# Kernel tuning notes

Measured on AMD Instinct MI355X. Metric: run time of the kernel, lower is better.

Reference implementation:

```python
import jax, jax.numpy as jnp
import numpy as np


def setup_inputs() -> dict:
    key = jax.random.key(0)
    k1, k2 = jax.random.split(key)
    B, C, H, W = 8, 128, 96, 160
    x1 = jax.random.normal(k1, (B, C, H, W), dtype=jnp.float32)
    x2 = jax.random.normal(k2, (B, C, H, W), dtype=jnp.float32)
    return {"x1": x1, "x2": x2, "d": 4}


def reference(x1, x2, d):
    # x1, x2: (B, C, H, W); output: (B, (2d+1)^2, H, W)
    b, c, h, w = x1.shape
    x2p = jnp.pad(x2, ((0, 0), (0, 0), (d, d), (d, d)))
    # Loop over the small fixed (2d+1)^2 displacement set (81 for d=4);
    # each term is a channel-reduced elementwise product (shift-multiply-sum).
    corrs = [
        jnp.einsum("bchw,bchw->bhw", x1,
                   jax.lax.dynamic_slice(x2p, (0, 0, i, j), (b, c, h, w)))
        for i in range(2 * d + 1)
        for j in range(2 * d + 1)
    ]
    out = jnp.stack(corrs, axis=1)  # (B, (2d+1)^2, H, W)
    return out / c
```

## Files before the change

kernel.cpp:

```cpp
#include <hip/hip_runtime.h>
#include <stdint.h>

#define Bb 8
#define Cc 128
#define Hh 96
#define Ww 160
#define HW (Hh*Ww)
#define Kk 81

typedef __attribute__((ext_vector_type(8))) short short8;
typedef __attribute__((ext_vector_type(4))) float floatx4;
typedef __attribute__((ext_vector_type(4))) unsigned int uintx4;

__device__ __forceinline__ uint32_t bf16rne(float f) {
  uint32_t u = __float_as_uint(f);
  return (u + 0x7FFFu + ((u >> 16) & 1u)) >> 16;
}


__global__ __launch_bounds__(512, 4)
void corr_kernel(const float* __restrict__ x1, const float* __restrict__ x2,
                 float* __restrict__ out) {
  __shared__ __align__(16) ushort ldsX2[16*24*40];
  __shared__ __align__(16) ushort ldsX1[8*16*40];

  const int tid = threadIdx.x;
  const int flat = blockIdx.x;
  const int b  = flat & 7;
  const int j  = flat >> 3;
  const int by = j / 10;
  const int bx = j - by * 10;
  const int w0 = bx * 16;
  const int h0 = by * 8;

  const int lane = tid & 63;
  const int wv   = tid >> 6;
  const int vy = wv & 3, vx = wv >> 2;
  const int n = lane & 15, quad = lane >> 4;
  const int s = n >> 3, pw = n & 7;

  floatx4 acc[10];
#pragma unroll
  for (int t = 0; t < 10; ++t) acc[t] = (floatx4){0.f, 0.f, 0.f, 0.f};

  for (int ck = 0; ck < 4; ++ck) {
    const int c0 = ck * 32;
    if (ck) __syncthreads();

#pragma unroll
    for (int it = 0; it < 3; ++it) {
      int T   = it * 512 + tid;
      int w24 = T % 24;
      int t2  = T / 24;
      int rw  = t2 & 15;
      int cg  = t2 >> 4;
      int gh = h0 - 4 + rw;
      int gw = w0 - 4 + w24;
      bool ok = ((unsigned)gh < Hh) && ((unsigned)gw < Ww);
      const float* src = x2 + ((size_t)(b*Cc + c0 + cg*8) * HW + gh*Ww + gw);
      uint32_t p0, p1, p2, p3;
      {
        float a0 = ok ? src[0*HW] : 0.f;
        float a1 = ok ? src[1*HW] : 0.f;
        float a2 = ok ? src[2*HW] : 0.f;
        float a3 = ok ? src[3*HW] : 0.f;
        float a4 = ok ? src[4*HW] : 0.f;
        float a5 = ok ? src[5*HW] : 0.f;
        float a6 = ok ? src[6*HW] : 0.f;
        float a7 = ok ? src[7*HW] : 0.f;
        p0 = bf16rne(a0) | (bf16rne(a1) << 16);
        p1 = bf16rne(a2) | (bf16rne(a3) << 16);
        p2 = bf16rne(a4) | (bf16rne(a5) << 16);
        p3 = bf16rne(a6) | (bf16rne(a7) << 16);
      }
      *(uintx4*)&ldsX2[(rw*24 + w24)*40 + cg*8] = (uintx4){p0, p1, p2, p3};
    }

    {
      int T  = tid;
      int wl = T & 15;
      int t2 = T >> 4;
      int rl = t2 & 7;
      int cg = t2 >> 3;
      const float* src = x1 + ((size_t)(b*Cc + c0 + cg*8) * HW
                               + (h0 + rl)*Ww + (w0 + wl));
      uint32_t p0, p1, p2, p3;
      float a0 = src[0*HW], a1 = src[1*HW], a2 = src[2*HW], a3 = src[3*HW];
      float a4 = src[4*HW], a5 = src[5*HW], a6 = src[6*HW], a7 = src[7*HW];
      p0 = bf16rne(a0) | (bf16rne(a1) << 16);
      p1 = bf16rne(a2) | (bf16rne(a3) << 16);
      p2 = bf16rne(a4) | (bf16rne(a5) << 16);
      p3 = bf16rne(a6) | (bf16rne(a7) << 16);
      *(uintx4*)&ldsX1[(rl*16 + wl)*40 + cg*8] = (uintx4){p0, p1, p2, p3};
    }

    __syncthreads();

    short8 bfrag = *(const short8*)&ldsX1[((2*vy + s)*16 + 8*vx + pw)*40 + quad*8];
#pragma unroll
    for (int t = 0; t < 10; ++t) {
      short8 afrag = *(const short8*)&ldsX2[((2*vy + t)*24 + 8*vx + n)*40 + quad*8];
      acc[t] = __builtin_amdgcn_mfma_f32_16x16x32_bf16(afrag, bfrag, acc[t], 0, 0, 0);
    }
  }

  const float scale = 1.0f / 128.0f;
  const int ph  = h0 + 2*vy + s;
  const int pwg = w0 + 8*vx + pw;
#pragma unroll
  for (int t = 0; t < 10; ++t) {
    int di = t - 4 - s;
    if ((unsigned)(di + 4) > 8u) continue;
#pragma unroll
    for (int r = 0; r < 4; ++r) {
      int dj = quad*4 + r - 4 - pw;
      if ((unsigned)(dj + 4) > 8u) continue;
      int kk = (di + 4) * 9 + (dj + 4);
      out[((size_t)b*Kk + kk) * HW + ph*Ww + pwg] = acc[t][r] * scale;
    }
  }
}

extern "C" void kernel_launch(void* const* d_in, const int* in_sizes, int n_in,
                              void* d_out, int out_size, void* d_ws, size_t ws_size,
                              hipStream_t stream) {
  const float* x1 = (const float*)d_in[0];
  const float* x2 = (const float*)d_in[1];
  float* out = (float*)d_out;
  corr_kernel<<<dim3(960, 1, 1), dim3(512, 1, 1), 0, stream>>>(x1, x2, out);
}
```

Baseline: 187.0 us.

## Pre-transpose inputs to bf16 channel-last in workspace, then correlate directly from global

Adds a transpose kernel that converts x1 and x2 from NCHW fp32 into NHWC bf16 in the workspace. A new correlation kernel then loads MFMA fragments straight from global memory as contiguous 16-byte channel vectors, without LDS staging or barriers. This removes the strided per-channel loads and repeated bf16 conversion of halo data in every block. In exchange it adds a second launch and a full extra read and write pass over both inputs. The path runs only when the workspace is large enough and otherwise falls back to the old kernel.

```diff
diff --git a/kernel.cpp b/kernel.cpp
--- a/kernel.cpp
+++ b/kernel.cpp
@@ -1,5 +1,6 @@
 #include <hip/hip_runtime.h>
 #include <stdint.h>
+#include <stddef.h>
 
 #define Bb 8
 #define Cc 128
@@ -17,6 +18,100 @@
   return (u + 0x7FFFu + ((u >> 16) & 1u)) >> 16;
 }
 
+
+#define TPX 32
+__global__ __launch_bounds__(256)
+void transpose_kernel(const float* __restrict__ x1, const float* __restrict__ x2,
+                      ushort* __restrict__ x1t, ushort* __restrict__ x2t) {
+  __shared__ float lds[TPX * 130];
+  const int t   = threadIdx.x;
+  const int b   = blockIdx.y;
+  const int hw0 = blockIdx.x * TPX;
+  const float* src = blockIdx.z ? x2 : x1;
+  ushort*      dst = blockIdx.z ? x2t : x1t;
+
+  const int p4 = t & 7;
+  const int cb = t >> 3;
+#pragma unroll
+  for (int i = 0; i < 4; ++i) {
+    const int c = cb + i * 32;
+    floatx4 v = *(const floatx4*)&src[(size_t)(b * Cc + c) * HW + hw0 + p4 * 4];
+#pragma unroll
+    for (int jj = 0; jj < 4; ++jj)
+      lds[(p4 * 4 + jj) * 130 + c] = v[jj];
+  }
+  __syncthreads();
+
+  const int px = t >> 3;
+#pragma unroll
+  for (int i = 0; i < 2; ++i) {
+    const int k = (t & 7) + 8 * i;
+    const float* row = &lds[px * 130 + k * 8];
+    uint32_t q0 = bf16rne(row[0]) | (bf16rne(row[1]) << 16);
+    uint32_t q1 = bf16rne(row[2]) | (bf16rne(row[3]) << 16);
+    uint32_t q2 = bf16rne(row[4]) | (bf16rne(row[5]) << 16);
+    uint32_t q3 = bf16rne(row[6]) | (bf16rne(row[7]) << 16);
+    *(uintx4*)&dst[((size_t)b * HW + hw0 + px) * Cc + k * 8] = (uintx4){q0, q1, q2, q3};
+  }
+}
+
+__global__ __launch_bounds__(512)
+void corr_t_kernel(const ushort* __restrict__ x1t, const ushort* __restrict__ x2t,
+                   float* __restrict__ out) {
+  const int tid  = threadIdx.x;
+  const int flat = blockIdx.x;
+  const int b  = flat & 7;
+  const int j  = flat >> 3;
+  const int by = j / 10;
+  const int bx = j - by * 10;
+  const int w0 = bx * 16;
+  const int h0 = by * 8;
+
+  const int lane = tid & 63;
+  const int wv   = tid >> 6;
+  const int vy = wv & 3, vx = wv >> 2;
+  const int n = lane & 15, quad = lane >> 4;
+  const int s = n >> 3, pw = n & 7;
+
+  floatx4 acc[10];
+#pragma unroll
+  for (int t = 0; t < 10; ++t) acc[t] = (floatx4){0.f, 0.f, 0.f, 0.f};
+
+  const int gw2  = w0 - 4 + 8 * vx + n;
+  const bool okw = (unsigned)gw2 < (unsigned)Ww;
+  const int gh2b = h0 - 4 + 2 * vy;
+  const long p2  = ((long)b * HW + (long)gh2b * Ww + gw2) * Cc;
+  const long p1  = ((long)b * HW + (long)(h0 + 2 * vy + s) * Ww
+                    + (w0 + 8 * vx + pw)) * Cc;
+
+#pragma unroll
+  for (int ck = 0; ck < 4; ++ck) {
+    const short8 bfrag = *(const short8*)&x1t[p1 + ck * 32 + quad * 8];
+#pragma unroll
+    for (int t = 0; t < 10; ++t) {
+      short8 afrag = (short8){0, 0, 0, 0, 0, 0, 0, 0};
+      if (okw && (unsigned)(gh2b + t) < (unsigned)Hh)
+        afrag = *(const short8*)&x2t[p2 + (long)t * (Ww * Cc) + ck * 32 + quad * 8];
+      acc[t] = __builtin_amdgcn_mfma_f32_16x16x32_bf16(afrag, bfrag, acc[t], 0, 0, 0);
+    }
+  }
+
+  const float scale = 1.0f / 128.0f;
+  const int ph  = h0 + 2 * vy + s;
+  const int pwg = w0 + 8 * vx + pw;
+#pragma unroll
+  for (int t = 0; t < 10; ++t) {
+    int di = t - 4 - s;
+    if ((unsigned)(di + 4) > 8u) continue;
+#pragma unroll
+    for (int r = 0; r < 4; ++r) {
+      int dj = quad * 4 + r - 4 - pw;
+      if ((unsigned)(dj + 4) > 8u) continue;
+      int kk = (di + 4) * 9 + (dj + 4);
+      out[((size_t)b * Kk + kk) * HW + ph * Ww + pwg] = acc[t][r] * scale;
+    }
+  }
+}
 
 __global__ __launch_bounds__(512, 4)
 void corr_kernel(const float* __restrict__ x1, const float* __restrict__ x2,
@@ -127,5 +222,17 @@
   const float* x1 = (const float*)d_in[0];
   const float* x2 = (const float*)d_in[1];
   float* out = (float*)d_out;
-  corr_kernel<<<dim3(960, 1, 1), dim3(512, 1, 1), 0, stream>>>(x1, x2, out);
-}
+
+  const size_t elems = (size_t)Bb * HW * Cc;
+  const size_t need  = 2 * elems * sizeof(ushort);
+
+  if (d_ws != nullptr && ws_size >= need) {
+    ushort* x1t = (ushort*)d_ws;
+    ushort* x2t = x1t + elems;
+    transpose_kernel<<<dim3(HW / TPX, Bb, 2), dim3(256, 1, 1), 0, stream>>>(
+        x1, x2, x1t, x2t);
+    corr_t_kernel<<<dim3(960, 1, 1), dim3(512, 1, 1), 0, stream>>>(x1t, x2t, out);
+  } else {
+    corr_kernel<<<dim3(960, 1, 1), dim3(512, 1, 1), 0, stream>>>(x1, x2, out);
+  }
+}
```

Result: slower. 224.5 us (+20.1%).
